# Kernel tuning notes

Hardware: AMD Instinct MI355X
Metric: run time of the kernel (lower is better)

Reference implementation:

```python
import jax, jax.numpy as jnp
import numpy as np

B, C, L, H, D = 2, 1024, 2048, 16, 64  # batch, n_factor, seq, heads, head_dim
LN_EPS = 1e-5


def setup_inputs() -> dict:
    key = jax.random.key(0)
    ks = jax.random.split(key, 8)
    s = 0.02
    return {
        "x": jax.random.normal(ks[0], (B, C, L), jnp.float32),
        "y": jax.random.normal(ks[1], (B, C, L), jnp.float32),
        "Wq": jax.random.normal(ks[2], (H, C, D), jnp.float32) * s,
        "Wk": jax.random.normal(ks[3], (H, C, D), jnp.float32) * s,
        "Wv": jax.random.normal(ks[4], (H, C, D), jnp.float32) * s,
        "bq": jax.random.normal(ks[5], (H, D), jnp.float32) * s,
        "bk": jax.random.normal(ks[6], (H, D), jnp.float32) * s,
        "bv": jax.random.normal(ks[7], (H, D), jnp.float32) * s,
        "gamma": jnp.ones((C,), jnp.float32),
        "beta": jnp.zeros((C,), jnp.float32),
    }


def reference(x, y, Wq, Wk, Wv, bq, bk, bv, gamma, beta):
    # Per-head Conv1d(kernel=1) == per-position linear; batch all heads at once.
    # x,y: [B, C, L]; W*: [H, C, D]; result q/k/v: [B, H, L, D]
    q = jnp.einsum('bcl,hcd->bhld', x, Wq) + bq[None, :, None, :]
    k = jnp.einsum('bcl,hcd->bhld', y, Wk) + bk[None, :, None, :]
    v = jnp.einsum('bcl,hcd->bhld', y, Wv) + bv[None, :, None, :]

    scale = 1.0 / jnp.sqrt(jnp.float32(D))  # n_factor_head ** 0.5
    scores = jnp.einsum('bhqd,bhkd->bhqk', q, k) * scale  # [B,H,L,L]
    attn = jax.nn.softmax(scores, axis=-1)
    ctx = jnp.einsum('bhqk,bhkd->bhqd', attn, v)  # [B,H,L,D]

    # torch.cat over heads along last dim == [B, L, H*D]
    att = jnp.transpose(ctx, (0, 2, 1, 3)).reshape(B, L, H * D)

    h = jnp.transpose(x, (0, 2, 1)) + att  # residual on x permuted to [B,L,C]
    mu = jnp.mean(h, axis=-1, keepdims=True)
    var = jnp.var(h, axis=-1, keepdims=True)
    out = (h - mu) * jax.lax.rsqrt(var + LN_EPS) * gamma + beta
    # dropout: identity in eval mode
    return out
```

## Files before the change

kernel.cpp:

```cpp
#include <hip/hip_runtime.h>
#include <hip/hip_bf16.h>

#define DEVI __device__ __forceinline__

typedef unsigned short u16;
typedef __bf16 bf16x8 __attribute__((ext_vector_type(8)));
typedef float f32x4 __attribute__((ext_vector_type(4)));

constexpr int Bn = 2, Cn = 1024, Ln = 2048, Hn = 16, Dn = 64;

DEVI u16 f2bfu(float f) { return __builtin_bit_cast(u16, __float2bfloat16(f)); }
DEVI float bfu2f(u16 u) { return __bfloat162float(__builtin_bit_cast(__hip_bfloat16, u)); }
DEVI f32x4 mfma16(bf16x8 a, bf16x8 b, f32x4 c) {
  return __builtin_amdgcn_mfma_f32_16x16x32_bf16(a, b, c, 0, 0, 0);
}
DEVI unsigned pk2(float lo, float hi) {
  return (unsigned)f2bfu(lo) | ((unsigned)f2bfu(hi) << 16);
}
DEVI void gld16(const u16* g, u16* l) {
  __builtin_amdgcn_global_load_lds(
      (const __attribute__((address_space(1))) unsigned*)g,
      (__attribute__((address_space(3))) unsigned*)l, 16, 0, 0);
}
DEVI int fsw(int row) { return (row & 7) ^ (((row >> 3) & 1) << 2); }

__global__ __launch_bounds__(256) void transpose_xy(const float* __restrict__ x,
                                                    const float* __restrict__ y,
                                                    u16* __restrict__ xT,
                                                    u16* __restrict__ yT) {
  int z = blockIdx.z;
  int which = z >> 1, b = z & 1;
  const float* src = (which ? y : x) + (size_t)b * Cn * Ln;
  u16* dst = (which ? yT : xT) + (size_t)b * Ln * Cn;
  int l0 = blockIdx.x * 64, c0 = blockIdx.y * 64;
  __shared__ float tile[64][65];
  int t = threadIdx.x;
  #pragma unroll
  for (int i = 0; i < 16; ++i) {
    int idx = i * 256 + t;
    int r = idx >> 6, cc = idx & 63;
    tile[r][cc] = src[(size_t)(c0 + r) * Ln + (l0 + cc)];
  }
  __syncthreads();
  #pragma unroll
  for (int i = 0; i < 8; ++i) {
    int idx = i * 256 + t;
    int r = idx >> 5, cc = (idx & 31) * 2;
    unsigned pkv = pk2(tile[cc][r], tile[cc + 1][r]);
    *(unsigned*)(&dst[(size_t)(l0 + r) * Cn + (c0 + cc)]) = pkv;
  }
}

__global__ __launch_bounds__(256) void transpose_w(const float* __restrict__ Wq,
                                                   const float* __restrict__ Wk,
                                                   const float* __restrict__ Wv,
                                                   u16* __restrict__ WT) {
  int c0 = blockIdx.x * 64, h = blockIdx.y, which = blockIdx.z;
  const float* src = (which == 0 ? Wq : (which == 1 ? Wk : Wv)) + (size_t)h * Cn * Dn;
  u16* dst = WT + ((size_t)which * Hn + h) * Dn * Cn;
  __shared__ float tile[64][65];
  int t = threadIdx.x;
  #pragma unroll
  for (int i = 0; i < 16; ++i) {
    int idx = i * 256 + t;
    int r = idx >> 6, cc = idx & 63;
    tile[r][cc] = src[(size_t)(c0 + r) * Dn + cc];
  }
  __syncthreads();
  #pragma unroll
  for (int i = 0; i < 16; ++i) {
    int idx = i * 256 + t;
    int r = idx >> 6, cc = idx & 63;
    dst[(size_t)r * Cn + (c0 + cc)] = f2bfu(tile[cc][r]);
  }
}

__global__ __launch_bounds__(256) void gemm_qkv3(const u16* __restrict__ xT,
                                                 const u16* __restrict__ yT,
                                                 const u16* __restrict__ WT,
                                                 const float* __restrict__ bq,
                                                 const float* __restrict__ bk,
                                                 const float* __restrict__ bv,
                                                 u16* __restrict__ Qb,
                                                 u16* __restrict__ Kb,
                                                 u16* __restrict__ Vt) {
  int mt = blockIdx.x, by = blockIdx.y, b = blockIdx.z;
  int which = by >> 3, hp = by & 7;
  const u16* A = (which == 0 ? xT : yT) + (size_t)b * Ln * Cn + (size_t)mt * 128 * Cn;
  const u16* Bw = WT + ((size_t)which * 1024 + (size_t)hp * 128) * Cn;
  __shared__ __align__(16) u16 smem[2 * 128 * 64];
  u16* lA = smem;
  u16* lB = smem + 128 * 64;
  int t = threadIdx.x, wave = t >> 6, lane = t & 63;
  int wr = wave >> 1, wc = wave & 1;
  int ml = lane & 15, kg = lane >> 4;
  f32x4 acc[4][4] = {};
  for (int k0 = 0; k0 < Cn; k0 += 64) {
    __syncthreads();
    #pragma unroll
    for (int j = 0; j < 4; ++j) {
      int q = wave * 256 + j * 64 + lane;
      int row = q >> 3, p = q & 7, c16 = p ^ (row & 7);
      gld16(A + (size_t)row * Cn + k0 + c16 * 8, &lA[(wave * 256 + j * 64) * 8]);
    }
    #pragma unroll
    for (int j = 0; j < 4; ++j) {
      int q = wave * 256 + j * 64 + lane;
      int row = q >> 3, p = q & 7, c16 = p ^ (row & 7);
      gld16(Bw + (size_t)row * Cn + k0 + c16 * 8, &lB[(wave * 256 + j * 64) * 8]);
    }
    __syncthreads();
    bf16x8 af[4][2], bf[4][2];
    #pragma unroll
    for (int m = 0; m < 4; ++m) {
      int row = wr * 64 + m * 16 + ml;
      #pragma unroll
      for (int kk = 0; kk < 2; ++kk) {
        int p = (kk * 4 + kg) ^ (row & 7);
        af[m][kk] = *(const bf16x8*)(&lA[row * 64 + p * 8]);
      }
    }
    #pragma unroll
    for (int n = 0; n < 4; ++n) {
      int row = wc * 64 + n * 16 + ml;
      #pragma unroll
      for (int kk = 0; kk < 2; ++kk) {
        int p = (kk * 4 + kg) ^ (row & 7);
        bf[n][kk] = *(const bf16x8*)(&lB[row * 64 + p * 8]);
      }
    }
    __builtin_amdgcn_s_setprio(1);
    #pragma unroll
    for (int m = 0; m < 4; ++m)
      #pragma unroll
      for (int n = 0; n < 4; ++n)
        #pragma unroll
        for (int kk = 0; kk < 2; ++kk)
          acc[m][n] = mfma16(af[m][kk], bf[n][kk], acc[m][n]);
    __builtin_amdgcn_s_setprio(0);
  }
  int head = hp * 2 + wc;
  const float* bp = (which == 0 ? bq : (which == 1 ? bk : bv));
  if (which < 2) {
    u16* O = (which == 0 ? Qb : Kb) + (((size_t)b * Hn + head) * Ln + (size_t)mt * 128) * Dn;
    #pragma unroll
    for (int n = 0; n < 4; ++n) {
      float bvv = bp[head * 64 + n * 16 + ml];
      #pragma unroll
      for (int m = 0; m < 4; ++m)
        #pragma unroll
        for (int r = 0; r < 4; ++r) {
          int row = wr * 64 + m * 16 + kg * 4 + r;
          O[(size_t)row * Dn + n * 16 + ml] = f2bfu(acc[m][n][r] + bvv);
        }
    }
  } else {
    __syncthreads();
    #pragma unroll
    for (int n = 0; n < 4; ++n) {
      float bvv = bp[head * 64 + n * 16 + ml];
      int n_loc = wc * 64 + n * 16 + ml;
      int swz = (n_loc & 7) << 4;
      #pragma unroll
      for (int m = 0; m < 4; ++m) {
        int m_base = wr * 64 + m * 16 + kg * 4;
        uint2 pkd;
        pkd.x = pk2(acc[m][n][0] + bvv, acc[m][n][1] + bvv);
        pkd.y = pk2(acc[m][n][2] + bvv, acc[m][n][3] + bvv);
        *(uint2*)(&smem[n_loc * 128 + (m_base ^ swz)]) = pkd;
      }
    }
    __syncthreads();
    u16* Vbase = Vt + ((size_t)b * Hn + hp * 2) * Dn * Ln + (size_t)mt * 128;
    #pragma unroll
    for (int i = 0; i < 8; ++i) {
      int chunk = i * 256 + t;
      int n = chunk >> 4, cc = chunk & 15;
      uint4 vv = *(const uint4*)(&smem[n * 128 + (cc ^ ((n & 7) << 1)) * 8]);
      *(uint4*)(Vbase + (size_t)n * Ln + cc * 8) = vv;
    }
  }
}

__global__ __launch_bounds__(256, 4) void flash_attn(const u16* __restrict__ Qg,
                                                     const u16* __restrict__ Kg,
                                                     const u16* __restrict__ Vtg,
                                                     u16* __restrict__ att) {
  int n = blockIdx.x + 32 * (blockIdx.y + 16 * blockIdx.z);
  int xcd = n & 7, m = n >> 3;
  int grp = xcd * 4 + (m >> 5);
  int qt = m & 31;
  int h = grp & 15, b = grp >> 4;

  size_t bh = (size_t)b * Hn + h;
  const u16* Qp = Qg + (bh * Ln + (size_t)qt * 64) * Dn;
  const u16* Kp = Kg + bh * Ln * Dn;
  const u16* Vp = Vtg + bh * Dn * Ln;
  int t = threadIdx.x, wave = t >> 6, lane = t & 63;
  int qs = wave & 1, g = wave >> 1;
  int ml = lane & 15, kg = lane >> 4;
  __shared__ __align__(16) u16 Kl[2][64 * 64];
  __shared__ __align__(16) u16 Vl[2][64 * 64];

  constexpr float QS = 0.125f * 1.44269504f;
  bf16x8 qf[2][2];
  #pragma unroll
  for (int qg = 0; qg < 2; ++qg)
    #pragma unroll
    for (int kk = 0; kk < 2; ++kk) {
      bf16x8 raw = *(const bf16x8*)(Qp + (size_t)(qs * 32 + qg * 16 + ml) * Dn + kk * 32 + kg * 8);
      #pragma unroll
      for (int j = 0; j < 8; ++j) raw[j] = (__bf16)((float)raw[j] * QS);
      qf[qg][kk] = raw;
    }

  f32x4 ctx[2][4] = {};
  float psum[2] = {0.f, 0.f};

  int koff[2][2], voff[4];
  {
    #pragma unroll
    for (int nt = 0; nt < 2; ++nt) {
      int rowk = g * 32 + 8 * (ml >> 2) + 4 * nt + (ml & 3);
      #pragma unroll
      for (int kk = 0; kk < 2; ++kk)
        koff[nt][kk] = rowk * 64 + (((kk * 4 + kg) ^ fsw(rowk)) << 3);
    }
    #pragma unroll
    for (int nt = 0; nt < 4; ++nt) {
      int rowv = nt * 16 + ml;
      voff[nt] = rowv * 64 + ((((g * 4 + kg) ^ fsw(rowv))) << 3);
    }
  }
  int row_st[2], c16_st[2];
  #pragma unroll
  for (int j = 0; j < 2; ++j) {
    int q = j * 256 + t;
    row_st[j] = q >> 3;
    c16_st[j] = ((q & 7) ^ fsw(row_st[j])) * 8;
  }

  auto stage = [&](int buf, int kv0) {
    #pragma unroll
    for (int j = 0; j < 2; ++j)
      gld16(Kp + (size_t)(kv0 + row_st[j]) * Dn + c16_st[j],
            &Kl[buf][(j * 256 + wave * 64) * 8]);
    #pragma unroll
    for (int j = 0; j < 2; ++j)
      gld16(Vp + (size_t)row_st[j] * Ln + kv0 + c16_st[j],
            &Vl[buf][(j * 256 + wave * 64) * 8]);
  };

  constexpr int NT = Ln / 64;

  auto tile = [&](int cur, int tt) {
    if (tt + 1 < NT) {
      stage(cur ^ 1, (tt + 1) * 64);
      asm volatile("s_waitcnt vmcnt(4)" ::: "memory");
    } else {
      asm volatile("s_waitcnt vmcnt(0)" ::: "memory");
    }
    __builtin_amdgcn_s_barrier();
    __builtin_amdgcn_sched_barrier(0);
    const u16* Kh = Kl[cur];
    const u16* Vh = Vl[cur];
    bf16x8 kf[2][2];
    #pragma unroll
    for (int nt = 0; nt < 2; ++nt)
      #pragma unroll
      for (int kk = 0; kk < 2; ++kk)
        kf[nt][kk] = *(const bf16x8*)(&Kh[koff[nt][kk]]);
    f32x4 s[2][2] = {};
    __builtin_amdgcn_s_setprio(1);
    #pragma unroll
    for (int nt = 0; nt < 2; ++nt)
      #pragma unroll
      for (int kk = 0; kk < 2; ++kk)
        #pragma unroll
        for (int qg = 0; qg < 2; ++qg)
          s[qg][nt] = mfma16(kf[nt][kk], qf[qg][kk], s[qg][nt]);
    __builtin_amdgcn_s_setprio(0);
    bf16x8 pf[2];
    #pragma unroll
    for (int qg = 0; qg < 2; ++qg) {
      f32x4 e0, e1;
      #pragma unroll
      for (int r = 0; r < 4; ++r) e0[r] = __builtin_amdgcn_exp2f(s[qg][0][r]);
      #pragma unroll
      for (int r = 0; r < 4; ++r) e1[r] = __builtin_amdgcn_exp2f(s[qg][1][r]);
      psum[qg] += (e0[0] + e0[1]) + (e0[2] + e0[3]) + (e1[0] + e1[1]) + (e1[2] + e1[3]);
      uint4 pw;
      pw.x = pk2(e0[0], e0[1]);
      pw.y = pk2(e0[2], e0[3]);
      pw.z = pk2(e1[0], e1[1]);
      pw.w = pk2(e1[2], e1[3]);
      pf[qg] = __builtin_bit_cast(bf16x8, pw);
    }
    __builtin_amdgcn_s_setprio(1);
    #pragma unroll
    for (int nt = 0; nt < 4; ++nt) {
      bf16x8 vf = *(const bf16x8*)(&Vh[voff[nt]]);
      #pragma unroll
      for (int qg = 0; qg < 2; ++qg)
        ctx[qg][nt] = mfma16(pf[qg], vf, ctx[qg][nt]);
    }
    __builtin_amdgcn_s_setprio(0);
    asm volatile("s_waitcnt lgkmcnt(0)" ::: "memory");
    __builtin_amdgcn_s_barrier();
  };

  stage(0, 0);
  asm volatile("s_waitcnt vmcnt(0)" ::: "memory");
  __builtin_amdgcn_s_barrier();

  for (int tt = 0; tt < NT; tt += 2) {
    tile(0, tt);
    tile(1, tt + 1);
  }

  __syncthreads();
  float* comb = (float*)&Kl[0][0];
  float* psA = (float*)&Vl[0][0];
  if (g == 1) {
    #pragma unroll
    for (int qg = 0; qg < 2; ++qg) {
      #pragma unroll
      for (int nt = 0; nt < 4; ++nt)
        #pragma unroll
        for (int r = 0; r < 4; ++r)
          comb[(((qs * 2 + qg) * 16) + nt * 4 + r) * 64 + lane] = ctx[qg][nt][r];
      psA[(qs * 2 + qg) * 64 + lane] = psum[qg];
    }
  }
  __syncthreads();
  if (g == 0) {
    #pragma unroll
    for (int qg = 0; qg < 2; ++qg) {
      #pragma unroll
      for (int nt = 0; nt < 4; ++nt)
        #pragma unroll
        for (int r = 0; r < 4; ++r)
          ctx[qg][nt][r] += comb[(((qs * 2 + qg) * 16) + nt * 4 + r) * 64 + lane];
      psum[qg] += psA[(qs * 2 + qg) * 64 + lane];
      psum[qg] += __shfl_xor(psum[qg], 16);
      psum[qg] += __shfl_xor(psum[qg], 32);
    }
    #pragma unroll
    for (int qg = 0; qg < 2; ++qg) {
      float inv[4];
      #pragma unroll
      for (int r = 0; r < 4; ++r) inv[r] = 1.f / __shfl(psum[qg], kg * 4 + r);
      #pragma unroll
      for (int nt = 0; nt < 4; ++nt)
        #pragma unroll
        for (int r = 0; r < 4; ++r) {
          size_t row = (size_t)b * Ln + qt * 64 + qs * 32 + qg * 16 + kg * 4 + r;
          att[row * Cn + h * Dn + nt * 16 + ml] = f2bfu(ctx[qg][nt][r] * inv[r]);
        }
    }
  }
}

__global__ __launch_bounds__(256) void ln_kernel(const u16* __restrict__ att,
                                                 const u16* __restrict__ xT,
                                                 const float* __restrict__ gamma,
                                                 const float* __restrict__ beta,
                                                 float* __restrict__ out) {
  size_t row = blockIdx.x;
  const u16* ap = att + row * Cn;
  const u16* xp = xT + row * Cn;
  float* op = out + row * Cn;
  int t = threadIdx.x;
  ushort4 a4 = *(const ushort4*)(ap + t * 4);
  ushort4 xv = *(const ushort4*)(xp + t * 4);
  float h0 = bfu2f(a4.x) + bfu2f(xv.x), h1 = bfu2f(a4.y) + bfu2f(xv.y);
  float h2 = bfu2f(a4.z) + bfu2f(xv.z), h3 = bfu2f(a4.w) + bfu2f(xv.w);
  float s = h0 + h1 + h2 + h3;
  float ss = h0 * h0 + h1 * h1 + h2 * h2 + h3 * h3;
  #pragma unroll
  for (int off = 1; off < 64; off <<= 1) {
    s += __shfl_xor(s, off);
    ss += __shfl_xor(ss, off);
  }
  __shared__ float red[8];
  int wave = t >> 6, lane = t & 63;
  if (lane == 0) { red[wave] = s; red[wave + 4] = ss; }
  __syncthreads();
  s = red[0] + red[1] + red[2] + red[3];
  ss = red[4] + red[5] + red[6] + red[7];
  float mu = s * (1.f / 1024.f);
  float var = ss * (1.f / 1024.f) - mu * mu;
  float rinv = rsqrtf(var + 1e-5f);
  float4 gmv = *(const float4*)(gamma + t * 4);
  float4 bev = *(const float4*)(beta + t * 4);
  float4 o;
  o.x = (h0 - mu) * rinv * gmv.x + bev.x;
  o.y = (h1 - mu) * rinv * gmv.y + bev.y;
  o.z = (h2 - mu) * rinv * gmv.z + bev.z;
  o.w = (h3 - mu) * rinv * gmv.w + bev.w;
  *(float4*)(op + t * 4) = o;
}

extern "C" void kernel_launch(void* const* d_in, const int* in_sizes, int n_in,
                              void* d_out, int out_size, void* d_ws, size_t ws_size,
                              hipStream_t stream) {
  const float* x = (const float*)d_in[0];
  const float* y = (const float*)d_in[1];
  const float* Wq = (const float*)d_in[2];
  const float* Wk = (const float*)d_in[3];
  const float* Wv = (const float*)d_in[4];
  const float* bq = (const float*)d_in[5];
  const float* bk = (const float*)d_in[6];
  const float* bv = (const float*)d_in[7];
  const float* gamma = (const float*)d_in[8];
  const float* beta = (const float*)d_in[9];
  float* out = (float*)d_out;

  char* ws = (char*)d_ws;
  u16* xT = (u16*)(ws + 0);
  u16* yT = (u16*)(ws + 8388608);
  u16* WT = (u16*)(ws + 16777216);
  u16* Qb = (u16*)(ws + 23068672);
  u16* Kb = (u16*)(ws + 31457280);
  u16* VT = (u16*)(ws + 39845888);
  u16* att = (u16*)(ws + 48234496);

  transpose_xy<<<dim3(Ln / 64, Cn / 64, 4), dim3(256), 0, stream>>>(x, y, xT, yT);
  transpose_w<<<dim3(Cn / 64, Hn, 3), dim3(256), 0, stream>>>(Wq, Wk, Wv, WT);
  gemm_qkv3<<<dim3(Ln / 128, 24, Bn), dim3(256), 0, stream>>>(xT, yT, WT, bq, bk, bv, Qb, Kb, VT);
  flash_attn<<<dim3(Ln / 64, Hn, Bn), dim3(256), 0, stream>>>(Qb, Kb, VT, att);
  ln_kernel<<<dim3(Bn * Ln), dim3(256), 0, stream>>>(att, xT, gamma, beta, out);
}
```

Baseline: 106.5 us.

## Software-pipeline QK and PV across tiles with four-deep K/V LDS ring

Restructures the flash-attention loop so the QK^T MFMAs of the next KV tile are issued alongside the exp/PV work of the previous tile, using alternating score registers and a 4-slot K/V LDS ring with prefetch one tile ahead. It also drops the trailing lgkmcnt wait and the per-tile end barrier. The aim is to hide exp and LDS latency behind MFMA work and to cut barriers. The cost is double LDS (64KB per block) and lower occupancy, with launch bounds dropped from 4 to 2 blocks.

```diff
diff --git a/kernel.cpp b/kernel.cpp
--- a/kernel.cpp
+++ b/kernel.cpp
@@ -182,7 +182,7 @@
   }
 }
 
-__global__ __launch_bounds__(256, 4) void flash_attn(const u16* __restrict__ Qg,
+__global__ __launch_bounds__(256, 2) void flash_attn(const u16* __restrict__ Qg,
                                                      const u16* __restrict__ Kg,
                                                      const u16* __restrict__ Vtg,
                                                      u16* __restrict__ att) {
@@ -199,8 +199,8 @@
   int t = threadIdx.x, wave = t >> 6, lane = t & 63;
   int qs = wave & 1, g = wave >> 1;
   int ml = lane & 15, kg = lane >> 4;
-  __shared__ __align__(16) u16 Kl[2][64 * 64];
-  __shared__ __align__(16) u16 Vl[2][64 * 64];
+  __shared__ __align__(16) u16 Kl[4][64 * 64];
+  __shared__ __align__(16) u16 Vl[4][64 * 64];
 
   constexpr float QS = 0.125f * 1.44269504f;
   bf16x8 qf[2][2];
@@ -251,35 +251,26 @@
             &Vl[buf][(j * 256 + wave * 64) * 8]);
   };
 
-  constexpr int NT = Ln / 64;
-
-  auto tile = [&](int cur, int tt) {
-    if (tt + 1 < NT) {
-      stage(cur ^ 1, (tt + 1) * 64);
-      asm volatile("s_waitcnt vmcnt(4)" ::: "memory");
-    } else {
-      asm volatile("s_waitcnt vmcnt(0)" ::: "memory");
-    }
-    __builtin_amdgcn_s_barrier();
-    __builtin_amdgcn_sched_barrier(0);
-    const u16* Kh = Kl[cur];
-    const u16* Vh = Vl[cur];
+  auto QK = [&](const u16* Kh, f32x4 (&s)[2][2]) {
     bf16x8 kf[2][2];
     #pragma unroll
     for (int nt = 0; nt < 2; ++nt)
       #pragma unroll
       for (int kk = 0; kk < 2; ++kk)
         kf[nt][kk] = *(const bf16x8*)(&Kh[koff[nt][kk]]);
-    f32x4 s[2][2] = {};
     __builtin_amdgcn_s_setprio(1);
     #pragma unroll
     for (int nt = 0; nt < 2; ++nt)
       #pragma unroll
-      for (int kk = 0; kk < 2; ++kk)
-        #pragma unroll
-        for (int qg = 0; qg < 2; ++qg)
-          s[qg][nt] = mfma16(kf[nt][kk], qf[qg][kk], s[qg][nt]);
+      for (int qg = 0; qg < 2; ++qg) {
+        f32x4 z = {};
+        s[qg][nt] = mfma16(kf[nt][0], qf[qg][0], z);
+        s[qg][nt] = mfma16(kf[nt][1], qf[qg][1], s[qg][nt]);
+      }
     __builtin_amdgcn_s_setprio(0);
+  };
+
+  auto PV = [&](const u16* Vh, f32x4 (&s)[2][2]) {
     bf16x8 pf[2];
     #pragma unroll
     for (int qg = 0; qg < 2; ++qg) {
@@ -305,18 +296,44 @@
         ctx[qg][nt] = mfma16(pf[qg], vf, ctx[qg][nt]);
     }
     __builtin_amdgcn_s_setprio(0);
-    asm volatile("s_waitcnt lgkmcnt(0)" ::: "memory");
+  };
+
+  constexpr int NT = Ln / 64;
+  f32x4 sA[2][2], sB[2][2];
+
+  stage(0, 0);
+  stage(1, 64);
+  asm volatile("s_waitcnt vmcnt(4)" ::: "memory");
+  __builtin_amdgcn_s_barrier();
+  __builtin_amdgcn_sched_barrier(0);
+  QK(&Kl[0][0], sA);
+
+  for (int tt = 1; tt < NT - 1; tt += 2) {
+    stage((tt + 1) & 3, (tt + 1) * 64);
+    asm volatile("s_waitcnt vmcnt(4)" ::: "memory");
     __builtin_amdgcn_s_barrier();
-  };
-
-  stage(0, 0);
+    __builtin_amdgcn_sched_barrier(0);
+    QK(&Kl[tt & 3][0], sB);
+    PV(&Vl[(tt - 1) & 3][0], sA);
+
+    if (tt + 2 < NT) {
+      stage((tt + 2) & 3, (tt + 2) * 64);
+      asm volatile("s_waitcnt vmcnt(4)" ::: "memory");
+    } else {
+      asm volatile("s_waitcnt vmcnt(0)" ::: "memory");
+    }
+    __builtin_amdgcn_s_barrier();
+    __builtin_amdgcn_sched_barrier(0);
+    QK(&Kl[(tt + 1) & 3][0], sA);
+    PV(&Vl[tt & 3][0], sB);
+  }
+
   asm volatile("s_waitcnt vmcnt(0)" ::: "memory");
   __builtin_amdgcn_s_barrier();
-
-  for (int tt = 0; tt < NT; tt += 2) {
-    tile(0, tt);
-    tile(1, tt + 1);
-  }
+  __builtin_amdgcn_sched_barrier(0);
+  QK(&Kl[(NT - 1) & 3][0], sB);
+  PV(&Vl[(NT - 2) & 3][0], sA);
+  PV(&Vl[(NT - 1) & 3][0], sB);
 
   __syncthreads();
   float* comb = (float*)&Kl[0][0];
```

Result: slower. 116.8 us (+9.7%).

## Enlarge QKV GEMM tiles to 256x256 with double-buffered LDS prefetch

Applied to the files above, without the earlier changes.

Replaces the 128x128 QKV projection GEMM with a 512-thread kernel that computes 256x256 output tiles and double-buffers the A/B k-slices in LDS. The next slice is prefetched via async global-to-LDS loads while MFMAs run on the current one. This increases operand reuse and hides load latency, but shrinks the grid to 192 blocks, which may leave compute units idle, and raises register and LDS pressure.

```diff
diff --git a/kernel.cpp b/kernel.cpp
--- a/kernel.cpp
+++ b/kernel.cpp
@@ -75,82 +75,112 @@
   }
 }
 
-__global__ __launch_bounds__(256) void gemm_qkv3(const u16* __restrict__ xT,
-                                                 const u16* __restrict__ yT,
-                                                 const u16* __restrict__ WT,
-                                                 const float* __restrict__ bq,
-                                                 const float* __restrict__ bk,
-                                                 const float* __restrict__ bv,
-                                                 u16* __restrict__ Qb,
-                                                 u16* __restrict__ Kb,
-                                                 u16* __restrict__ Vt) {
-  int mt = blockIdx.x, by = blockIdx.y, b = blockIdx.z;
-  int which = by >> 3, hp = by & 7;
-  const u16* A = (which == 0 ? xT : yT) + (size_t)b * Ln * Cn + (size_t)mt * 128 * Cn;
-  const u16* Bw = WT + ((size_t)which * 1024 + (size_t)hp * 128) * Cn;
-  __shared__ __align__(16) u16 smem[2 * 128 * 64];
-  u16* lA = smem;
-  u16* lB = smem + 128 * 64;
+__global__ __launch_bounds__(512, 2) void gemm256(const u16* __restrict__ xT,
+                                                  const u16* __restrict__ yT,
+                                                  const u16* __restrict__ WT,
+                                                  const float* __restrict__ bq,
+                                                  const float* __restrict__ bk,
+                                                  const float* __restrict__ bv,
+                                                  u16* __restrict__ Qb,
+                                                  u16* __restrict__ Kb,
+                                                  u16* __restrict__ Vt) {
+  int mt = blockIdx.x, by = blockIdx.y;
+  int which = by >> 2, hp = by & 3;
+  int b = mt >> 3, l0 = (mt & 7) * 256;
+  const u16* A = (which == 0 ? xT : yT) + (size_t)mt * 256 * Cn;
+  const u16* Bw = WT + ((size_t)which * 1024 + (size_t)hp * 256) * Cn;
+  __shared__ __align__(16) u16 smem[4 * 256 * 64];
   int t = threadIdx.x, wave = t >> 6, lane = t & 63;
-  int wr = wave >> 1, wc = wave & 1;
+  int wr = wave >> 2, wc = wave & 3;
   int ml = lane & 15, kg = lane >> 4;
-  f32x4 acc[4][4] = {};
-  for (int k0 = 0; k0 < Cn; k0 += 64) {
-    __syncthreads();
+  f32x4 acc[8][4] = {};
+
+  auto stage = [&](int buf, int k0) {
+    u16* la = smem + buf * 16384;
+    u16* lb = smem + 32768 + buf * 16384;
     #pragma unroll
     for (int j = 0; j < 4; ++j) {
-      int q = wave * 256 + j * 64 + lane;
-      int row = q >> 3, p = q & 7, c16 = p ^ (row & 7);
-      gld16(A + (size_t)row * Cn + k0 + c16 * 8, &lA[(wave * 256 + j * 64) * 8]);
+      int slot = j * 512 + t;
+      int row = slot >> 3, p = slot & 7, c16 = p ^ (row & 7);
+      gld16(A + (size_t)row * Cn + k0 + c16 * 8, la + (j * 512 + wave * 64) * 8);
     }
     #pragma unroll
     for (int j = 0; j < 4; ++j) {
-      int q = wave * 256 + j * 64 + lane;
-      int row = q >> 3, p = q & 7, c16 = p ^ (row & 7);
-      gld16(Bw + (size_t)row * Cn + k0 + c16 * 8, &lB[(wave * 256 + j * 64) * 8]);
-    }
-    __syncthreads();
-    bf16x8 af[4][2], bf[4][2];
-    #pragma unroll
-    for (int m = 0; m < 4; ++m) {
-      int row = wr * 64 + m * 16 + ml;
+      int slot = j * 512 + t;
+      int row = slot >> 3, p = slot & 7, c16 = p ^ (row & 7);
+      gld16(Bw + (size_t)row * Cn + k0 + c16 * 8, lb + (j * 512 + wave * 64) * 8);
+    }
+  };
+
+  stage(0, 0);
+  stage(1, 64);
+  asm volatile("s_waitcnt vmcnt(8)" ::: "memory");
+  __builtin_amdgcn_s_barrier();
+  __builtin_amdgcn_sched_barrier(0);
+
+  constexpr int NK = Cn / 64;
+  for (int tk = 0; tk < NK; ++tk) {
+    int cur = tk & 1;
+    if (tk >= 1) {
+      if (tk + 1 < NK) {
+        stage(cur ^ 1, (tk + 1) * 64);
+        asm volatile("s_waitcnt vmcnt(8)" ::: "memory");
+      } else {
+        asm volatile("s_waitcnt vmcnt(0)" ::: "memory");
+      }
+      __builtin_amdgcn_s_barrier();
+      __builtin_amdgcn_sched_barrier(0);
+    }
+    const u16* La = smem + cur * 16384;
+    const u16* Lb = smem + 32768 + cur * 16384;
+    bf16x8 bf[4][2];
+    #pragma unroll
+    for (int n = 0; n < 4; ++n) {
+      int row = wc * 64 + n * 16 + ml;
       #pragma unroll
       for (int kk = 0; kk < 2; ++kk) {
         int p = (kk * 4 + kg) ^ (row & 7);
-        af[m][kk] = *(const bf16x8*)(&lA[row * 64 + p * 8]);
+        bf[n][kk] = *(const bf16x8*)(&Lb[row * 64 + p * 8]);
       }
     }
     #pragma unroll
-    for (int n = 0; n < 4; ++n) {
-      int row = wc * 64 + n * 16 + ml;
-      #pragma unroll
-      for (int kk = 0; kk < 2; ++kk) {
-        int p = (kk * 4 + kg) ^ (row & 7);
-        bf[n][kk] = *(const bf16x8*)(&lB[row * 64 + p * 8]);
+    for (int mq = 0; mq < 4; ++mq) {
+      bf16x8 af[2][2];
+      #pragma unroll
+      for (int m2 = 0; m2 < 2; ++m2) {
+        int row = wr * 128 + mq * 32 + m2 * 16 + ml;
+        #pragma unroll
+        for (int kk = 0; kk < 2; ++kk) {
+          int p = (kk * 4 + kg) ^ (row & 7);
+          af[m2][kk] = *(const bf16x8*)(&La[row * 64 + p * 8]);
+        }
       }
-    }
-    __builtin_amdgcn_s_setprio(1);
-    #pragma unroll
-    for (int m = 0; m < 4; ++m)
-      #pragma unroll
-      for (int n = 0; n < 4; ++n)
-        #pragma unroll
-        for (int kk = 0; kk < 2; ++kk)
-          acc[m][n] = mfma16(af[m][kk], bf[n][kk], acc[m][n]);
-    __builtin_amdgcn_s_setprio(0);
-  }
-  int head = hp * 2 + wc;
+      __builtin_amdgcn_s_setprio(1);
+      #pragma unroll
+      for (int m2 = 0; m2 < 2; ++m2)
+        #pragma unroll
+        for (int n = 0; n < 4; ++n)
+          #pragma unroll
+          for (int kk = 0; kk < 2; ++kk)
+            acc[mq * 2 + m2][n] = mfma16(af[m2][kk], bf[n][kk], acc[mq * 2 + m2][n]);
+      __builtin_amdgcn_s_setprio(0);
+    }
+    asm volatile("s_waitcnt lgkmcnt(0)" ::: "memory");
+    __builtin_amdgcn_s_barrier();
+  }
+
+  int head = hp * 4 + wc;
   const float* bp = (which == 0 ? bq : (which == 1 ? bk : bv));
   if (which < 2) {
-    u16* O = (which == 0 ? Qb : Kb) + (((size_t)b * Hn + head) * Ln + (size_t)mt * 128) * Dn;
+    u16* O = (which == 0 ? Qb : Kb) + (((size_t)b * Hn + head) * Ln + l0) * Dn;
     #pragma unroll
     for (int n = 0; n < 4; ++n) {
       float bvv = bp[head * 64 + n * 16 + ml];
       #pragma unroll
-      for (int m = 0; m < 4; ++m)
+      for (int m = 0; m < 8; ++m)
         #pragma unroll
         for (int r = 0; r < 4; ++r) {
-          int row = wr * 64 + m * 16 + kg * 4 + r;
+          int row = wr * 128 + m * 16 + kg * 4 + r;
           O[(size_t)row * Dn + n * 16 + ml] = f2bfu(acc[m][n][r] + bvv);
         }
     }
@@ -162,22 +192,22 @@
       int n_loc = wc * 64 + n * 16 + ml;
       int swz = (n_loc & 7) << 4;
       #pragma unroll
-      for (int m = 0; m < 4; ++m) {
-        int m_base = wr * 64 + m * 16 + kg * 4;
+      for (int m = 0; m < 8; ++m) {
+        int l_base = wr * 128 + m * 16 + kg * 4;
         uint2 pkd;
         pkd.x = pk2(acc[m][n][0] + bvv, acc[m][n][1] + bvv);
         pkd.y = pk2(acc[m][n][2] + bvv, acc[m][n][3] + bvv);
-        *(uint2*)(&smem[n_loc * 128 + (m_base ^ swz)]) = pkd;
+        *(uint2*)(&smem[n_loc * 256 + (l_base ^ swz)]) = pkd;
       }
     }
     __syncthreads();
-    u16* Vbase = Vt + ((size_t)b * Hn + hp * 2) * Dn * Ln + (size_t)mt * 128;
-    #pragma unroll
-    for (int i = 0; i < 8; ++i) {
-      int chunk = i * 256 + t;
-      int n = chunk >> 4, cc = chunk & 15;
-      uint4 vv = *(const uint4*)(&smem[n * 128 + (cc ^ ((n & 7) << 1)) * 8]);
-      *(uint4*)(Vbase + (size_t)n * Ln + cc * 8) = vv;
+    u16* Vbase = Vt + (((size_t)b * Hn + hp * 4) * Dn) * Ln + l0;
+    #pragma unroll
+    for (int j = 0; j < 16; ++j) {
+      int chunk = j * 512 + t;
+      int n = chunk >> 5, lc = chunk & 31;
+      uint4 vv = *(const uint4*)(&smem[n * 256 + ((lc * 8) ^ ((n & 7) << 4))]);
+      *(uint4*)(Vbase + (size_t)n * Ln + lc * 8) = vv;
     }
   }
 }
@@ -427,7 +457,7 @@
 
   transpose_xy<<<dim3(Ln / 64, Cn / 64, 4), dim3(256), 0, stream>>>(x, y, xT, yT);
   transpose_w<<<dim3(Cn / 64, Hn, 3), dim3(256), 0, stream>>>(Wq, Wk, Wv, WT);
-  gemm_qkv3<<<dim3(Ln / 128, 24, Bn), dim3(256), 0, stream>>>(xT, yT, WT, bq, bk, bv, Qb, Kb, VT);
+  gemm256<<<dim3(16, 12), dim3(512), 0, stream>>>(xT, yT, WT, bq, bk, bv, Qb, Kb, VT);
   flash_attn<<<dim3(Ln / 64, Hn, Bn), dim3(256), 0, stream>>>(Qb, Kb, VT, att);
   ln_kernel<<<dim3(Bn * Ln), dim3(256), 0, stream>>>(att, xT, gamma, beta, out);
 }
```

Measured after the change: 104.6 us, median of 2. No clear change (-1.8%).
